# Optimization experiments

Measured on AMD Instinct MI355X. Metric: run time of the kernel, lower is better.

Reference implementation:

```python
import jax, jax.numpy as jnp
import numpy as np

B, S, D = 8, 2048, 128

def setup_inputs() -> dict:
    key = jax.random.key(0)
    kq, kk, kv = jax.random.split(key, 3)
    return {
        "query": jax.random.normal(kq, (B, S, D), dtype=jnp.float32),
        "key": jax.random.normal(kk, (B, S, D), dtype=jnp.float32),
        "value": jax.random.normal(kv, (B, S, D), dtype=jnp.float32),
    }

def reference(query, key, value):
    # softmax(QK^T / sqrt(d_k)) V, no mask, dropout=0
    d_k = query.shape[-1]
    scale = 1.0 / np.sqrt(d_k).astype(np.float32)
    # [B, Sq, Sk]
    attn_scores = jnp.einsum('bqd,bkd->bqk', query, key) * scale
    attn_weights = jax.nn.softmax(attn_scores, axis=-1)
    # [B, Sq, Dv]
    output = jnp.einsum('bqk,bkd->bqd', attn_weights, value)
    return (output, attn_weights)
```

## Files before the change

### kernel.cpp

```cpp
#include <hip/hip_runtime.h>
#include <hip/hip_bf16.h>

#define NB 8
#define SS 2048
#define DD 128
#define NQK (NB * SS * DD)

typedef __attribute__((ext_vector_type(8))) short bf16x8;
typedef __attribute__((ext_vector_type(16))) float f32x16;
typedef __attribute__((ext_vector_type(4))) float f32x4;
typedef __attribute__((ext_vector_type(4))) unsigned int uint4v;
typedef __attribute__((ext_vector_type(2))) unsigned int uint2v;

static constexpr float C1 = 0.08838834764831845f * 1.4426950408889634f;

#define MFMA32(a, b, c) __builtin_amdgcn_mfma_f32_32x32x16_bf16(a, b, c, 0, 0, 0)
#define PSWAP(a, b) __builtin_amdgcn_permlane32_swap(a, b, false, false)

#if __has_builtin(__builtin_amdgcn_exp2f)
#define EXP2 __builtin_amdgcn_exp2f
#else
#define EXP2 exp2f
#endif

__device__ __forceinline__ unsigned short f2bf(float x) {
  __hip_bfloat16 h = __float2bfloat16(x);
  unsigned short r;
  __builtin_memcpy(&r, &h, 2);
  return r;
}

__device__ __forceinline__ void nt_store4(const float* src, float* dst) {
  f32x4 v;
  __builtin_memcpy(&v, src, 16);
  __builtin_nontemporal_store(v, (f32x4*)dst);
}

__global__ __launch_bounds__(256)
void prep_kernel(const float* __restrict__ Q, const float* __restrict__ K,
                 const float* __restrict__ V, unsigned short* __restrict__ Qt,
                 unsigned short* __restrict__ Kt, unsigned short* __restrict__ Vt) {
  __shared__ __align__(16) float Tf[32][132];
  const int ti = blockIdx.x, b = blockIdx.y, role = blockIdx.z;
  const int tid = threadIdx.x;
  const float* src = role == 0 ? Q : (role == 1 ? K : V);
  {
    const int row = tid >> 3, seg = (tid & 7) * 16;
    const float4* sp = (const float4*)(src + ((size_t)b * SS + ti * 32 + row) * DD + seg);
#pragma unroll
    for (int j = 0; j < 4; ++j) *(float4*)&Tf[row][seg + 4 * j] = sp[j];
  }
  __syncthreads();
  if (role < 2) {
    unsigned short* dst = (role == 0 ? Qt : Kt) + ((size_t)b * 64 + ti) * 4096;
#pragma unroll
    for (int e = 0; e < 2; ++e) {
      const int c = 2 * tid + e, lq = c & 31, ck = c >> 5;
      const float4 a = *(const float4*)&Tf[lq][ck * 8];
      const float4 d = *(const float4*)&Tf[lq][ck * 8 + 4];
      bf16x8 o;
      o[0] = (short)f2bf(a.x); o[1] = (short)f2bf(a.y);
      o[2] = (short)f2bf(a.z); o[3] = (short)f2bf(a.w);
      o[4] = (short)f2bf(d.x); o[5] = (short)f2bf(d.y);
      o[6] = (short)f2bf(d.z); o[7] = (short)f2bf(d.w);
      *(bf16x8*)(dst + c * 8) = o;
    }
  } else {
    unsigned short* dst = Vt + ((size_t)b * 64 + ti) * 4096;
#pragma unroll
    for (int e = 0; e < 2; ++e) {
      const int chunk = 2 * tid + e, cc = chunk >> 7, d = chunk & 127;
      bf16x8 o;
#pragma unroll
      for (int j = 0; j < 8; ++j) o[j] = (short)f2bf(Tf[cc * 8 + j][d]);
      *(bf16x8*)(dst + chunk * 8) = o;
    }
  }
}

__global__ __launch_bounds__(256, 3)
void stats_kernel(const unsigned short* __restrict__ Qt,
                  const unsigned short* __restrict__ Kt,
                  float2* __restrict__ partials) {
  const int b = blockIdx.z, qb = blockIdx.x, ks = blockIdx.y;
  const int tid = threadIdx.x;
  const int lane = tid & 63, wv = tid >> 6;
  const int lq = lane & 31, h2 = lane >> 5;
  const int q0t = qb * 4 + wv;
  const f32x16 ZERO16 = {0, 0, 0, 0, 0, 0, 0, 0, 0, 0, 0, 0, 0, 0, 0, 0};

  const unsigned short* qbase = Qt + ((size_t)b * 64 + q0t) * 4096;
  bf16x8 qh[8];
#pragma unroll
  for (int ds = 0; ds < 8; ++ds)
    qh[ds] = *(const bf16x8*)(qbase + ((ds * 2 + h2) * 32 + lq) * 8);

  float m2 = -1e30f, s2 = 0.f;
#pragma unroll
  for (int kp = 0; kp < 2; ++kp) {
    const unsigned short* kb0 = Kt + ((size_t)b * 64 + ks * 4 + 2 * kp) * 4096;
    const unsigned short* kb1 = kb0 + 4096;
    bf16x8 a0[8], a1[8];
#pragma unroll
    for (int ds = 0; ds < 8; ++ds) {
      a0[ds] = *(const bf16x8*)(kb0 + ((ds * 2 + h2) * 32 + lq) * 8);
      a1[ds] = *(const bf16x8*)(kb1 + ((ds * 2 + h2) * 32 + lq) * 8);
    }
    f32x16 acc0 = ZERO16, acc1 = ZERO16;
#pragma unroll
    for (int ds = 0; ds < 8; ++ds) {
      acc0 = MFMA32(a0[ds], qh[ds], acc0);
      acc1 = MFMA32(a1[ds], qh[ds], acc1);
    }
    float tm0 = acc0[0], tm1 = acc1[0];
#pragma unroll
    for (int r = 1; r < 16; ++r) {
      tm0 = fmaxf(tm0, acc0[r]);
      tm1 = fmaxf(tm1, acc1[r]);
    }
    const float nm2 = fmaxf(m2, fmaxf(tm0, tm1) * C1);
    float add = 0.f;
#pragma unroll
    for (int r = 0; r < 16; ++r)
      add += EXP2(fmaf(acc0[r], C1, -nm2)) + EXP2(fmaf(acc1[r], C1, -nm2));
    s2 = s2 * EXP2(m2 - nm2) + add;
    m2 = nm2;
  }
  const float mo = __shfl_xor(m2, 32);
  const float so = __shfl_xor(s2, 32);
  const float nm = fmaxf(m2, mo);
  s2 = s2 * EXP2(m2 - nm) + so * EXP2(mo - nm);
  if (h2 == 0)
    partials[((size_t)b * SS + q0t * 32 + lq) * 16 + ks] = make_float2(nm, s2);
}

__global__ __launch_bounds__(256, 2)
void fused_kernel(const unsigned short* __restrict__ Qt,
                  const unsigned short* __restrict__ Kt,
                  const unsigned short* __restrict__ Vt,
                  const float2* __restrict__ partials,
                  float* __restrict__ W, float* __restrict__ Out) {
  __shared__ __align__(16) float PW[4][32][40];
  __shared__ __align__(16) float R[32][132];
  __shared__ float lbs[32];

  const int b = blockIdx.y, qb = blockIdx.x;
  const int q0 = qb * 32;
  const int tid = threadIdx.x;
  const int lane = tid & 63, wv = tid >> 6;
  const int lq = lane & 31, h2 = lane >> 5;
  const f32x16 ZERO16 = {0, 0, 0, 0, 0, 0, 0, 0, 0, 0, 0, 0, 0, 0, 0, 0};

  if (tid < 32) {
    const float2* pp = partials + ((size_t)b * SS + q0 + tid) * 16;
    float2 p[16];
    float m = -1e30f;
#pragma unroll
    for (int j = 0; j < 16; ++j) {
      p[j] = pp[j];
      m = fmaxf(m, p[j].x);
    }
    float s = 0.f;
#pragma unroll
    for (int j = 0; j < 16; ++j) s += p[j].y * EXP2(p[j].x - m);
    lbs[tid] = -(m + __log2f(s));
  }
  {
    float* Rf = &R[0][0];
    for (int idx = tid; idx < 32 * 132; idx += 256) Rf[idx] = 0.f;
  }
  __syncthreads();

  const unsigned short* qbase = Qt + ((size_t)b * 64 + (q0 >> 5)) * 4096;
  bf16x8 qh[8];
#pragma unroll
  for (int ds = 0; ds < 8; ++ds)
    qh[ds] = *(const bf16x8*)(qbase + ((ds * 2 + h2) * 32 + lq) * 8);
  const float lb = lbs[lq];

  float* pwwr[4];
#pragma unroll
  for (int g = 0; g < 4; ++g)
    pwwr[g] = &PW[wv][lq][(8 * g + 4 * h2 + lq * 4) & 31];
  const int gq8 = lane >> 3, gks = lane & 7;
  const float* pwrd[4];
  float* wgb[4];
#pragma unroll
  for (int i = 0; i < 4; ++i) {
    const int row = i * 8 + gq8;
    pwrd[i] = &PW[wv][row][(gks * 4 + row * 4) & 31];
    wgb[i] = W + ((size_t)b * SS + q0 + row) * SS + gks * 4;
  }

  f32x16 accO[4];
#pragma unroll
  for (int dt = 0; dt < 4; ++dt) accO[dt] = ZERO16;

  const unsigned short* const ktw = Kt + ((size_t)b * 64 + wv * 16) * 4096;
  const unsigned short* const vtw = Vt + ((size_t)b * 64 + wv * 16) * 4096;

  f32x16 acc = ZERO16;
  bf16x8 vb[8];
  {
    bf16x8 ah[8];
#pragma unroll
    for (int ds = 0; ds < 8; ++ds)
      ah[ds] = *(const bf16x8*)(ktw + ((ds * 2 + h2) * 32 + lq) * 8);
#pragma unroll
    for (int ds = 0; ds < 8; ++ds) acc = MFMA32(ah[ds], qh[ds], acc);
#pragma unroll
    for (int kk = 0; kk < 2; ++kk)
#pragma unroll
      for (int dt = 0; dt < 4; ++dt)
        vb[kk * 4 + dt] =
            *(const bf16x8*)(vtw + ((kk * 2 + h2) * 128 + dt * 32 + lq) * 8);
  }

  for (int kt = 0; kt < 16; ++kt) {
    const int kb = (wv * 16 + kt) * 32;
    bf16x8 ahn[8], vbn[8];
    if (kt < 15) {
      const unsigned short* kn = ktw + (kt + 1) * 4096;
      const unsigned short* vn = vtw + (kt + 1) * 4096;
#pragma unroll
      for (int ds = 0; ds < 8; ++ds)
        ahn[ds] = *(const bf16x8*)(kn + ((ds * 2 + h2) * 32 + lq) * 8);
#pragma unroll
      for (int kk = 0; kk < 2; ++kk)
#pragma unroll
        for (int dt = 0; dt < 4; ++dt)
          vbn[kk * 4 + dt] =
              *(const bf16x8*)(vn + ((kk * 2 + h2) * 128 + dt * 32 + lq) * 8);
    }
    unsigned int U[8];
#pragma unroll
    for (int g = 0; g < 4; ++g) {
      const float p0 = EXP2(fmaf(acc[4 * g + 0], C1, lb));
      const float p1 = EXP2(fmaf(acc[4 * g + 1], C1, lb));
      const float p2 = EXP2(fmaf(acc[4 * g + 2], C1, lb));
      const float p3 = EXP2(fmaf(acc[4 * g + 3], C1, lb));
      *(float4*)pwwr[g] = make_float4(p0, p1, p2, p3);
      U[2 * g] = (unsigned)f2bf(p0) | ((unsigned)f2bf(p1) << 16);
      U[2 * g + 1] = (unsigned)f2bf(p2) | ((unsigned)f2bf(p3) << 16);
    }
    f32x16 accn = ZERO16;
    if (kt < 15) {
#pragma unroll
      for (int ds = 0; ds < 8; ++ds) accn = MFMA32(ahn[ds], qh[ds], accn);
    }
#pragma unroll
    for (int i = 0; i < 4; ++i) nt_store4(pwrd[i], wgb[i] + kb);
    const uint2v s02 = PSWAP(U[0], U[2]);
    const uint2v s13 = PSWAP(U[1], U[3]);
    const uint2v s46 = PSWAP(U[4], U[6]);
    const uint2v s57 = PSWAP(U[5], U[7]);
    uint4v w0, w1;
    w0.x = s02.x; w0.y = s13.x; w0.z = s02.y; w0.w = s13.y;
    w1.x = s46.x; w1.y = s57.x; w1.z = s46.y; w1.w = s57.y;
    const bf16x8 pa0 = __builtin_bit_cast(bf16x8, w0);
    const bf16x8 pa1 = __builtin_bit_cast(bf16x8, w1);
#pragma unroll
    for (int dt = 0; dt < 4; ++dt) accO[dt] = MFMA32(pa0, vb[dt], accO[dt]);
#pragma unroll
    for (int dt = 0; dt < 4; ++dt) accO[dt] = MFMA32(pa1, vb[4 + dt], accO[dt]);
    acc = accn;
#pragma unroll
    for (int j = 0; j < 8; ++j) vb[j] = vbn[j];
  }

  __syncthreads();
#pragma unroll
  for (int ph = 0; ph < 4; ++ph) {
    if (wv == ph) {
#pragma unroll
      for (int dt = 0; dt < 4; ++dt) {
#pragma unroll
        for (int r = 0; r < 16; ++r) {
          const int q = (r & 3) + 8 * (r >> 2) + 4 * h2;
          R[q][dt * 32 + lq] += accO[dt][r];
        }
      }
    }
    __syncthreads();
  }
  {
    const int row = tid >> 3, c0 = (tid & 7) * 16;
    float* ob = Out + ((size_t)b * SS + q0 + row) * DD + c0;
#pragma unroll
    for (int j = 0; j < 4; ++j) nt_store4(&R[row][c0 + 4 * j], ob + 4 * j);
  }
}

extern "C" void kernel_launch(void* const* d_in, const int* in_sizes, int n_in,
                              void* d_out, int out_size, void* d_ws, size_t ws_size,
                              hipStream_t stream) {
  const float* Q = (const float*)d_in[0];
  const float* K = (const float*)d_in[1];
  const float* V = (const float*)d_in[2];
  float* out = (float*)d_out;
  float* W = out + (size_t)NQK;

  char* ws = (char*)d_ws;
  unsigned short* Qt = (unsigned short*)(ws);
  unsigned short* Kt = (unsigned short*)(ws + ((size_t)4 << 20));
  unsigned short* Vt = (unsigned short*)(ws + ((size_t)8 << 20));
  float2* partials = (float2*)(ws + ((size_t)12 << 20));

  prep_kernel<<<dim3(64, 8, 3), 256, 0, stream>>>(Q, K, V, Qt, Kt, Vt);
  stats_kernel<<<dim3(16, 16, 8), 256, 0, stream>>>(Qt, Kt, partials);
  fused_kernel<<<dim3(64, 8), 256, 0, stream>>>(Qt, Kt, Vt, partials, W, out);
}
```

Measured before the change: 72.82 us.

## Fuse softmax statistics pass into the attention kernel, dropping stats launch

```diff
diff --git a/kernel.cpp b/kernel.cpp
--- a/kernel.cpp
+++ b/kernel.cpp
@@ -78,71 +78,14 @@
   }
 }
 
-__global__ __launch_bounds__(256, 3)
-void stats_kernel(const unsigned short* __restrict__ Qt,
-                  const unsigned short* __restrict__ Kt,
-                  float2* __restrict__ partials) {
-  const int b = blockIdx.z, qb = blockIdx.x, ks = blockIdx.y;
-  const int tid = threadIdx.x;
-  const int lane = tid & 63, wv = tid >> 6;
-  const int lq = lane & 31, h2 = lane >> 5;
-  const int q0t = qb * 4 + wv;
-  const f32x16 ZERO16 = {0, 0, 0, 0, 0, 0, 0, 0, 0, 0, 0, 0, 0, 0, 0, 0};
-
-  const unsigned short* qbase = Qt + ((size_t)b * 64 + q0t) * 4096;
-  bf16x8 qh[8];
-#pragma unroll
-  for (int ds = 0; ds < 8; ++ds)
-    qh[ds] = *(const bf16x8*)(qbase + ((ds * 2 + h2) * 32 + lq) * 8);
-
-  float m2 = -1e30f, s2 = 0.f;
-#pragma unroll
-  for (int kp = 0; kp < 2; ++kp) {
-    const unsigned short* kb0 = Kt + ((size_t)b * 64 + ks * 4 + 2 * kp) * 4096;
-    const unsigned short* kb1 = kb0 + 4096;
-    bf16x8 a0[8], a1[8];
-#pragma unroll
-    for (int ds = 0; ds < 8; ++ds) {
-      a0[ds] = *(const bf16x8*)(kb0 + ((ds * 2 + h2) * 32 + lq) * 8);
-      a1[ds] = *(const bf16x8*)(kb1 + ((ds * 2 + h2) * 32 + lq) * 8);
-    }
-    f32x16 acc0 = ZERO16, acc1 = ZERO16;
-#pragma unroll
-    for (int ds = 0; ds < 8; ++ds) {
-      acc0 = MFMA32(a0[ds], qh[ds], acc0);
-      acc1 = MFMA32(a1[ds], qh[ds], acc1);
-    }
-    float tm0 = acc0[0], tm1 = acc1[0];
-#pragma unroll
-    for (int r = 1; r < 16; ++r) {
-      tm0 = fmaxf(tm0, acc0[r]);
-      tm1 = fmaxf(tm1, acc1[r]);
-    }
-    const float nm2 = fmaxf(m2, fmaxf(tm0, tm1) * C1);
-    float add = 0.f;
-#pragma unroll
-    for (int r = 0; r < 16; ++r)
-      add += EXP2(fmaf(acc0[r], C1, -nm2)) + EXP2(fmaf(acc1[r], C1, -nm2));
-    s2 = s2 * EXP2(m2 - nm2) + add;
-    m2 = nm2;
-  }
-  const float mo = __shfl_xor(m2, 32);
-  const float so = __shfl_xor(s2, 32);
-  const float nm = fmaxf(m2, mo);
-  s2 = s2 * EXP2(m2 - nm) + so * EXP2(mo - nm);
-  if (h2 == 0)
-    partials[((size_t)b * SS + q0t * 32 + lq) * 16 + ks] = make_float2(nm, s2);
-}
-
 __global__ __launch_bounds__(256, 2)
-void fused_kernel(const unsigned short* __restrict__ Qt,
-                  const unsigned short* __restrict__ Kt,
-                  const unsigned short* __restrict__ Vt,
-                  const float2* __restrict__ partials,
-                  float* __restrict__ W, float* __restrict__ Out) {
+void attn_kernel(const unsigned short* __restrict__ Qt,
+                 const unsigned short* __restrict__ Kt,
+                 const unsigned short* __restrict__ Vt,
+                 float* __restrict__ W, float* __restrict__ Out) {
   __shared__ __align__(16) float PW[4][32][40];
   __shared__ __align__(16) float R[32][132];
-  __shared__ float lbs[32];
+  __shared__ float2 sms[4][32];
 
   const int b = blockIdx.y, qb = blockIdx.x;
   const int q0 = qb * 32;
@@ -151,32 +94,73 @@
   const int lq = lane & 31, h2 = lane >> 5;
   const f32x16 ZERO16 = {0, 0, 0, 0, 0, 0, 0, 0, 0, 0, 0, 0, 0, 0, 0, 0};
 
-  if (tid < 32) {
-    const float2* pp = partials + ((size_t)b * SS + q0 + tid) * 16;
-    float2 p[16];
-    float m = -1e30f;
-#pragma unroll
-    for (int j = 0; j < 16; ++j) {
-      p[j] = pp[j];
-      m = fmaxf(m, p[j].x);
-    }
-    float s = 0.f;
-#pragma unroll
-    for (int j = 0; j < 16; ++j) s += p[j].y * EXP2(p[j].x - m);
-    lbs[tid] = -(m + __log2f(s));
-  }
   {
     float* Rf = &R[0][0];
     for (int idx = tid; idx < 32 * 132; idx += 256) Rf[idx] = 0.f;
   }
-  __syncthreads();
 
   const unsigned short* qbase = Qt + ((size_t)b * 64 + (q0 >> 5)) * 4096;
   bf16x8 qh[8];
 #pragma unroll
   for (int ds = 0; ds < 8; ++ds)
     qh[ds] = *(const bf16x8*)(qbase + ((ds * 2 + h2) * 32 + lq) * 8);
-  const float lb = lbs[lq];
+
+  const unsigned short* const ktw = Kt + ((size_t)b * 64 + wv * 16) * 4096;
+  const unsigned short* const vtw = Vt + ((size_t)b * 64 + wv * 16) * 4096;
+
+  float m2 = -1e30f, s2 = 0.f;
+#pragma unroll
+  for (int kp = 0; kp < 8; ++kp) {
+    const unsigned short* kb0 = ktw + (2 * kp) * 4096;
+    const unsigned short* kb1 = kb0 + 4096;
+    bf16x8 a0[8], a1[8];
+#pragma unroll
+    for (int ds = 0; ds < 8; ++ds) {
+      a0[ds] = *(const bf16x8*)(kb0 + ((ds * 2 + h2) * 32 + lq) * 8);
+      a1[ds] = *(const bf16x8*)(kb1 + ((ds * 2 + h2) * 32 + lq) * 8);
+    }
+    f32x16 acc0 = ZERO16, acc1 = ZERO16;
+#pragma unroll
+    for (int ds = 0; ds < 8; ++ds) {
+      acc0 = MFMA32(a0[ds], qh[ds], acc0);
+      acc1 = MFMA32(a1[ds], qh[ds], acc1);
+    }
+    float tm0 = acc0[0], tm1 = acc1[0];
+#pragma unroll
+    for (int r = 1; r < 16; ++r) {
+      tm0 = fmaxf(tm0, acc0[r]);
+      tm1 = fmaxf(tm1, acc1[r]);
+    }
+    const float nm2 = fmaxf(m2, fmaxf(tm0, tm1) * C1);
+    float add = 0.f;
+#pragma unroll
+    for (int r = 0; r < 16; ++r)
+      add += EXP2(fmaf(acc0[r], C1, -nm2)) + EXP2(fmaf(acc1[r], C1, -nm2));
+    s2 = s2 * EXP2(m2 - nm2) + add;
+    m2 = nm2;
+  }
+  {
+    const float mo = __shfl_xor(m2, 32);
+    const float so = __shfl_xor(s2, 32);
+    const float nm = fmaxf(m2, mo);
+    s2 = s2 * EXP2(m2 - nm) + so * EXP2(mo - nm);
+    if (h2 == 0) sms[wv][lq] = make_float2(nm, s2);
+  }
+  __syncthreads();
+  float lb;
+  {
+    float2 pj[4];
+    float m = -1e30f;
+#pragma unroll
+    for (int j = 0; j < 4; ++j) {
+      pj[j] = sms[j][lq];
+      m = fmaxf(m, pj[j].x);
+    }
+    float s = 0.f;
+#pragma unroll
+    for (int j = 0; j < 4; ++j) s += pj[j].y * EXP2(pj[j].x - m);
+    lb = -(m + __log2f(s));
+  }
 
   float* pwwr[4];
 #pragma unroll
@@ -195,9 +179,6 @@
   f32x16 accO[4];
 #pragma unroll
   for (int dt = 0; dt < 4; ++dt) accO[dt] = ZERO16;
-
-  const unsigned short* const ktw = Kt + ((size_t)b * 64 + wv * 16) * 4096;
-  const unsigned short* const vtw = Vt + ((size_t)b * 64 + wv * 16) * 4096;
 
   f32x16 acc = ZERO16;
   bf16x8 vb[8];
@@ -304,9 +285,7 @@
   unsigned short* Qt = (unsigned short*)(ws);
   unsigned short* Kt = (unsigned short*)(ws + ((size_t)4 << 20));
   unsigned short* Vt = (unsigned short*)(ws + ((size_t)8 << 20));
-  float2* partials = (float2*)(ws + ((size_t)12 << 20));
 
   prep_kernel<<<dim3(64, 8, 3), 256, 0, stream>>>(Q, K, V, Qt, Kt, Vt);
-  stats_kernel<<<dim3(16, 16, 8), 256, 0, stream>>>(Qt, Kt, partials);
-  fused_kernel<<<dim3(64, 8), 256, 0, stream>>>(Qt, Kt, Vt, partials, W, out);
-}
+  attn_kernel<<<dim3(64, 8), 256, 0, stream>>>(Qt, Kt, Vt, W, out);
+}
```

Measured after the change: 66.60 us. 1.09x faster.
